# Optimization experiments

Measured on AMD Instinct MI355X. Metric: run time of the kernel, lower is better.

The kernel has to match this reference:

```python
import jax, jax.numpy as jnp
import numpy as np

B, L, D = 128, 512, 768   # batch, bert tokens, bert hidden
J = 32                    # clause boundaries -> S = J + 1 segments
S = J + 1
DM, DF = 200, 200         # transformer d_model / ffn dim
EPS = 1e-5


def _ln(x, g, b):
    m = x.mean(-1, keepdims=True)
    v = ((x - m) ** 2).mean(-1, keepdims=True)
    return (x - m) / jnp.sqrt(v + EPS) * g + b


def setup_inputs() -> dict:
    key = jax.random.key(0)
    ks = jax.random.split(key, 12)
    sc = 0.02
    hidden_state = jax.random.normal(ks[0], (B, L, D), jnp.float32)
    # strictly increasing, positive clause boundaries < L (non-empty segments)
    seg = L // S  # stride ~= 15 tokens per clause
    jitter = jax.random.randint(ks[1], (B, J), 0, seg).astype(jnp.int32)
    clause_idx = jnp.arange(1, J + 1, dtype=jnp.int32)[None, :] * seg + jitter
    p = lambda k, shp: sc * jax.random.normal(k, shp, jnp.float32)
    z = lambda n: jnp.zeros((n,), jnp.float32)
    return {
        'hidden_state': hidden_state,
        'clause_idx': clause_idx,
        'fc5_w': p(ks[2], (1, D)), 'fc5_b': z(1),
        'fc1_w': p(ks[3], (DM, D)), 'fc1_b': z(DM),
        'attn_in_w': p(ks[4], (3 * DM, DM)), 'attn_in_b': z(3 * DM),
        'attn_out_w': p(ks[5], (DM, DM)), 'attn_out_b': z(DM),
        'ln1_g': jnp.ones((DM,), jnp.float32), 'ln1_b': z(DM),
        'lin1_w': p(ks[6], (DF, DM)), 'lin1_b': z(DF),
        'lin2_w': p(ks[7], (DM, DF)), 'lin2_b': z(DM),
        'ln2_g': jnp.ones((DM,), jnp.float32), 'ln2_b': z(DM),
        'fc_w': p(ks[8], (2, 2 * DM)), 'fc_b': z(2),
    }


def reference(hidden_state, clause_idx, fc5_w, fc5_b, fc1_w, fc1_b,
              attn_in_w, attn_in_b, attn_out_w, attn_out_b,
              ln1_g, ln1_b, lin1_w, lin1_b, lin2_w, lin2_b,
              ln2_g, ln2_b, fc_w, fc_b):
    # ---- ragged per-segment attention pooling (batched_index_select) ----
    t = jnp.arange(L)
    # segment id of each token: number of boundaries <= t  -> [B, L] in [0, S)
    seg_id = jnp.sum(t[None, None, :] >= clause_idx[:, :, None], axis=1)
    scores = jnp.einsum('bld,d->bl', hidden_state, fc5_w[0]) + fc5_b[0]  # fc5
    mask = seg_id[:, None, :] == jnp.arange(S)[None, :, None]            # [B,S,L]
    logits = jnp.where(mask, scores[:, None, :], -jnp.inf)
    w = jax.nn.softmax(logits, axis=-1)        # per-segment softmax over tokens
    pooled = jnp.einsum('bsl,bld->bsd', w, hidden_state)                 # [B,S,D]

    # ---- fc1 + TransformerEncoderLayer (post-norm, 1 head, relu, no dropout)
    x = pooled @ fc1_w.T + fc1_b                                         # [B,S,DM]
    qkv = x @ attn_in_w.T + attn_in_b
    q, k, v = jnp.split(qkv, 3, axis=-1)
    a = jax.nn.softmax(jnp.einsum('bqd,bkd->bqk', q, k) * (1.0 / np.sqrt(DM).item()), axis=-1)
    att = jnp.einsum('bqk,bkd->bqd', a, v) @ attn_out_w.T + attn_out_b
    x = _ln(x + att, ln1_g, ln1_b)
    ff = jax.nn.relu(x @ lin1_w.T + lin1_b) @ lin2_w.T + lin2_b
    x = _ln(x + ff, ln2_g, ln2_b)

    # ---- cat(first-token broadcast, rest) then classifier fc ----
    h = jnp.concatenate([jnp.broadcast_to(x[:, :1, :], (B, S - 1, DM)), x[:, 1:, :]], axis=-1)
    return h @ fc_w.T + fc_b                                             # [B, S-1, 2]
```

## Files before the change

kernel.cpp:

```cpp
#include <hip/hip_runtime.h>

#define NB 128
#define LL 512
#define DD 768
#define JJ 32
#define SS 33
#define DM 200

typedef __attribute__((ext_vector_type(8))) short bf8_t;
typedef __attribute__((ext_vector_type(4))) float f4_t;

#define SB_XF   0
#define SB_QB   61440
#define SB_KB   82944
#define SB_VT   104448
#define SB_AB   131072
#define SB_Y2   235520
#define SB_BLK  275456

static __device__ __forceinline__ unsigned short f2bf(float f) {
  unsigned u = __float_as_uint(f);
  return (unsigned short)((u + 0x7FFFu + ((u >> 16) & 1u)) >> 16);
}

template<int KS>
static __device__ __forceinline__ f4_t mfma_tile(
    const unsigned short* pa, const unsigned short* pw)
{
  f4_t acc = {0.f, 0.f, 0.f, 0.f};
  bf8_t a = *(const bf8_t*)pa;
  bf8_t w = *(const bf8_t*)pw;
#pragma unroll
  for (int s = 1; s < KS; ++s) {
    bf8_t a2 = *(const bf8_t*)(pa + 32 * s);
    bf8_t w2 = *(const bf8_t*)(pw + 32 * s);
    acc = __builtin_amdgcn_mfma_f32_16x16x32_bf16(a, w, acc, 0, 0, 0);
    a = a2; w = w2;
  }
  acc = __builtin_amdgcn_mfma_f32_16x16x32_bf16(a, w, acc, 0, 0, 0);
  return acc;
}

template<int KS, int LDA>
static __device__ __forceinline__ f4_t mfma_tile_lds(
    const unsigned short* pa, const unsigned short* pw)
{
  f4_t acc = {0.f, 0.f, 0.f, 0.f};
#pragma unroll
  for (int s = 0; s < KS; ++s) {
    bf8_t a = *(const bf8_t*)(pa + 32 * s);
    bf8_t w = *(const bf8_t*)(pw + 32 * s);
    acc = __builtin_amdgcn_mfma_f32_16x16x32_bf16(a, w, acc, 0, 0, 0);
  }
  return acc;
}

__global__ __launch_bounds__(512) void pc_kernel(
    const float* __restrict__ hidden, const int* __restrict__ clause,
    const float* __restrict__ fc5w, unsigned short* __restrict__ pooled_bf,
    const float* __restrict__ fc1_w, const float* __restrict__ ain_w,
    const float* __restrict__ aout_w, const float* __restrict__ lin1_w,
    const float* __restrict__ lin2_w,
    unsigned short* __restrict__ fc1_wb, unsigned short* __restrict__ ain_wb,
    unsigned short* __restrict__ aout_wb, unsigned short* __restrict__ lin1_wb,
    unsigned short* __restrict__ lin2_wb, char* __restrict__ scratch)
{
  const int tid = threadIdx.x;
  if (blockIdx.x >= NB * SS) {
    int t = (blockIdx.x - NB * SS) * 512 + tid;
    if (t < 208 * 768) {
      int n = t / 768, k = t - n * 768;
      fc1_wb[t] = f2bf((n < 200) ? fc1_w[n * 768 + k] : 0.f);
      return;
    }
    t -= 208 * 768;
    if (t < 608 * 224) {
      int n = t / 224, k = t - n * 224;
      ain_wb[t] = f2bf((n < 600 && k < 200) ? ain_w[n * 200 + k] : 0.f);
      return;
    }
    t -= 608 * 224;
    if (t < 208 * 224) {
      int n = t / 224, k = t - n * 224;
      aout_wb[t] = f2bf((n < 200 && k < 200) ? aout_w[n * 200 + k] : 0.f);
      return;
    }
    t -= 208 * 224;
    if (t < 208 * 224) {
      int n = t / 224, k = t - n * 224;
      lin1_wb[t] = f2bf((n < 200 && k < 200) ? lin1_w[n * 200 + k] : 0.f);
      return;
    }
    t -= 208 * 224;
    if (t < 208 * 224) {
      int n = t / 224, k = t - n * 224;
      lin2_wb[t] = f2bf((n < 200 && k < 200) ? lin2_w[n * 200 + k] : 0.f);
      return;
    }
    t -= 208 * 224;
    if (t < NB * 1408) {
      int b = t / 1408, r = t - b * 1408;
      char* sb = scratch + (size_t)b * SB_BLK;
      const uint4 z = make_uint4(0, 0, 0, 0);
      if (r < 576) {
        int bi = r / 192, rr = r - bi * 192;
        int row = rr >> 2, c = rr & 3;
        int off = (bi == 0) ? SB_QB : (bi == 1 ? SB_KB : SB_AB);
        *(uint4*)((unsigned short*)(sb + off) + row * 224 + 192 + c * 8) = z;
      } else {
        int rr = r - 576;
        int row = rr >> 2, c = rr & 3;
        *(uint4*)((unsigned short*)(sb + SB_VT) + row * 64 + 32 + c * 8) = z;
      }
    }
    return;
  }

  int blk = blockIdx.x;
  int b = blk / SS;
  int s = blk - b * SS;
  int t0 = (s == 0) ? 0 : clause[b * JJ + s - 1];
  int t1 = (s == JJ) ? LL : clause[b * JJ + s];
  int nt = t1 - t0;
  if (nt > 64) nt = 64;
  if (nt < 1) nt = 1;

  __shared__ float wsm[64];
  int wave = tid >> 6, lane = tid & 63;

  const float4* w4 = (const float4*)fc5w;
  for (int t = t0 + wave; t < t0 + nt; t += 8) {
    const float4* hp = (const float4*)(hidden + ((long long)b * LL + t) * DD);
    float acc = 0.f;
#pragma unroll
    for (int i = 0; i < 3; ++i) {
      float4 h = hp[lane + 64 * i];
      float4 w = w4[lane + 64 * i];
      acc += h.x * w.x + h.y * w.y + h.z * w.z + h.w * w.w;
    }
#pragma unroll
    for (int off = 32; off; off >>= 1) acc += __shfl_xor(acc, off);
    if (lane == 0) wsm[t - t0] = acc;
  }
  __syncthreads();

  if (wave == 0) {
    float v = (lane < nt) ? wsm[lane] : -__builtin_inff();
    float mx = v;
#pragma unroll
    for (int off = 32; off; off >>= 1) mx = fmaxf(mx, __shfl_xor(mx, off));
    float e = (lane < nt) ? __expf(v - mx) : 0.f;
    float sm = e;
#pragma unroll
    for (int off = 32; off; off >>= 1) sm += __shfl_xor(sm, off);
    if (lane < nt) wsm[lane] = e / sm;
  }
  __syncthreads();

  if (tid < 384) {
    const float2* base = (const float2*)(hidden + ((long long)b * LL + t0) * DD);
    float2 acc = make_float2(0.f, 0.f);
#pragma unroll 4
    for (int t = 0; t < nt; ++t) {
      float w = wsm[t];
      float2 h = base[t * 384 + tid];
      acc.x = fmaf(w, h.x, acc.x);
      acc.y = fmaf(w, h.y, acc.y);
    }
    ushort2 o;
    o.x = f2bf(acc.x); o.y = f2bf(acc.y);
    *(ushort2*)(pooled_bf + (long long)blk * DD + tid * 2) = o;
  }
}

__global__ __launch_bounds__(256) void k_fc1qkv(
    const unsigned short* __restrict__ pooled,
    const unsigned short* __restrict__ fc1_wb, const float* __restrict__ fc1_b,
    const unsigned short* __restrict__ ain_wb, const float* __restrict__ ain_b,
    char* __restrict__ scratch)
{
  const int b = blockIdx.x / 3, mt = blockIdx.x % 3, m0 = mt * 16;
  const int tid = threadIdx.x, wv = tid >> 6, lane = tid & 63;
  const int col = lane & 15, quad = lane >> 4, koff = quad * 8;

  char* sb = scratch + (size_t)b * SB_BLK;
  float* x_f32 = (float*)(sb + SB_XF);
  unsigned short* q_bf  = (unsigned short*)(sb + SB_QB);
  unsigned short* k_bf  = (unsigned short*)(sb + SB_KB);
  unsigned short* vt_bf = (unsigned short*)(sb + SB_VT);

  __shared__ __align__(16) unsigned short xb[16][232];
  for (int u = tid; u < 16 * 16; u += 256) {
    int row = u >> 4, c = u & 15;
    ((unsigned*)&xb[row][200])[c] = 0u;
  }

  const unsigned short* Ab = pooled + (size_t)b * SS * DD;
  for (int t = wv; t < 13; t += 4) {
    int n0 = t * 16;
    f4_t acc = mfma_tile<24>(Ab + (size_t)(m0 + col) * DD + koff,
                             fc1_wb + (size_t)(n0 + col) * DD + koff);
    int gn = n0 + col;
    if (gn < DM) {
      float bv = fc1_b[gn];
#pragma unroll
      for (int r = 0; r < 4; ++r) {
        int row = quad * 4 + r;
        float v = acc[r] + bv;
        x_f32[(m0 + row) * 208 + gn] = v;
        xb[row][gn] = f2bf(v);
      }
    }
  }
  __syncthreads();

  for (int t = wv; t < 38; t += 4) {
    int n0 = t * 16;
    f4_t acc = mfma_tile_lds<7, 232>(&xb[0][0] + col * 232 + koff,
                                     ain_wb + (size_t)(n0 + col) * 224 + koff);
    int gn = n0 + col;
    if (gn < 600) {
      float bv = ain_b[gn];
#pragma unroll
      for (int r = 0; r < 4; ++r) {
        int gm = m0 + quad * 4 + r;
        unsigned short bfv = f2bf(acc[r] + bv);
        if (gn < 200)      q_bf[gm * 224 + gn] = bfv;
        else if (gn < 400) k_bf[gm * 224 + (gn - 200)] = bfv;
        else if (gm < SS)  vt_bf[(gn - 400) * 64 + gm] = bfv;
      }
    }
  }
}

__global__ __launch_bounds__(512) void k_attn(char* __restrict__ scratch)
{
  const int b = blockIdx.x, tid = threadIdx.x;
  const int wv = tid >> 6, lane = tid & 63;
  const int col = lane & 15, quad = lane >> 4, koff = quad * 8;

  char* sb = scratch + (size_t)b * SB_BLK;
  const unsigned short* q_bf  = (const unsigned short*)(sb + SB_QB);
  const unsigned short* k_bf  = (const unsigned short*)(sb + SB_KB);
  const unsigned short* vt_bf = (const unsigned short*)(sb + SB_VT);
  unsigned short* att_bf = (unsigned short*)(sb + SB_AB);

  __shared__ __align__(16) char smem[16896];
  float*          sc = (float*)smem;
  unsigned short* Pb = (unsigned short*)(smem + 9984);

  for (int t = wv; t < 9; t += 8) {
    int mt = t / 3, nt = t - mt * 3;
    int m0 = mt * 16, n0 = nt * 16;
    f4_t acc = mfma_tile<7>(q_bf + (m0 + col) * 224 + koff,
                            k_bf + (n0 + col) * 224 + koff);
    int gn = n0 + col;
#pragma unroll
    for (int r = 0; r < 4; ++r)
      sc[(m0 + quad * 4 + r) * 52 + gn] = acc[r] * 0.07071067811865475f;
  }
  __syncthreads();

  if (tid < SS) {
    float mx = -1e30f;
    for (int j = 0; j < SS; ++j) mx = fmaxf(mx, sc[tid * 52 + j]);
    float sm = 0.f;
    for (int j = 0; j < SS; ++j) { float e = __expf(sc[tid * 52 + j] - mx); sc[tid * 52 + j] = e; sm += e; }
    float inv = 1.f / sm;
    for (int j = 0; j < SS; ++j) sc[tid * 52 + j] *= inv;
  }
  __syncthreads();
  for (int u = tid; u < 48 * 64; u += 512) {
    int m = u >> 6, k = u & 63;
    Pb[m * 72 + k] = (m < SS && k < SS) ? f2bf(sc[m * 52 + k]) : (unsigned short)0;
  }
  __syncthreads();

  for (int t = wv; t < 3 * 13; t += 8) {
    int mt = t / 13, nt = t - mt * 13;
    int m0 = mt * 16, n0 = nt * 16;
    f4_t acc = mfma_tile_lds<2, 72>(Pb + (m0 + col) * 72 + koff,
                                    vt_bf + (n0 + col) * 64 + koff);
    int gn = n0 + col;
    if (gn < DM) {
#pragma unroll
      for (int r = 0; r < 4; ++r)
        att_bf[(m0 + quad * 4 + r) * 224 + gn] = f2bf(acc[r]);
    }
  }
}

__global__ __launch_bounds__(256) void k_post(
    const unsigned short* __restrict__ aout_wb, const float* __restrict__ aout_b,
    const float* __restrict__ ln1_g, const float* __restrict__ ln1_b,
    const unsigned short* __restrict__ lin1_wb, const float* __restrict__ lin1_b,
    const unsigned short* __restrict__ lin2_wb, const float* __restrict__ lin2_b,
    const float* __restrict__ ln2_g, const float* __restrict__ ln2_b,
    char* __restrict__ scratch)
{
  const int b = blockIdx.x / 3, mt = blockIdx.x % 3, m0 = mt * 16;
  const int tid = threadIdx.x, wv = tid >> 6, lane = tid & 63;
  const int col = lane & 15, quad = lane >> 4, koff = quad * 8;

  char* sb = scratch + (size_t)b * SB_BLK;
  const unsigned short* att_bf = (const unsigned short*)(sb + SB_AB);
  const float* x_f32 = (const float*)(sb + SB_XF);
  float* y2g = (float*)(sb + SB_Y2);

  __shared__ float tc[16][211];
  __shared__ __align__(16) unsigned short yb[16][232];
  __shared__ __align__(16) unsigned short fb[16][232];
  for (int u = tid; u < 16 * 16; u += 256) {
    int row = u >> 4, c = u & 15;
    ((unsigned*)&yb[row][200])[c] = 0u;
    ((unsigned*)&fb[row][200])[c] = 0u;
  }

  for (int t = wv; t < 13; t += 4) {
    int n0 = t * 16;
    f4_t acc = mfma_tile<7>(att_bf + (m0 + col) * 224 + koff,
                            aout_wb + (size_t)(n0 + col) * 224 + koff);
    int gn = n0 + col;
    float bv = (gn < DM) ? aout_b[gn] : 0.f;
#pragma unroll
    for (int r = 0; r < 4; ++r) {
      int row = quad * 4 + r;
      float v = acc[r] + bv;
      if (gn < DM) v += x_f32[(m0 + row) * 208 + gn];
      tc[row][gn] = v;
    }
  }
  __syncthreads();

  for (int r = wv; r < 16; r += 4) {
    float* p = &tc[r][0];
    float vals[4]; float s = 0.f;
#pragma unroll
    for (int i = 0; i < 4; ++i) { int k = lane + 64 * i; vals[i] = (k < DM) ? p[k] : 0.f; s += vals[i]; }
#pragma unroll
    for (int off = 32; off; off >>= 1) s += __shfl_xor(s, off);
    float mean = s * (1.f / DM);
    float vs = 0.f;
#pragma unroll
    for (int i = 0; i < 4; ++i) { int k = lane + 64 * i; if (k < DM) { float d = vals[i] - mean; vs += d * d; } }
#pragma unroll
    for (int off = 32; off; off >>= 1) vs += __shfl_xor(vs, off);
    float rstd = rsqrtf(vs * (1.f / DM) + 1e-5f);
#pragma unroll
    for (int i = 0; i < 4; ++i) {
      int k = lane + 64 * i;
      if (k < DM) {
        float o = (vals[i] - mean) * rstd * ln1_g[k] + ln1_b[k];
        p[k] = o;
        yb[r][k] = f2bf(o);
      }
    }
  }
  __syncthreads();

  for (int t = wv; t < 13; t += 4) {
    int n0 = t * 16;
    f4_t acc = mfma_tile_lds<7, 232>(&yb[0][0] + col * 232 + koff,
                                     lin1_wb + (size_t)(n0 + col) * 224 + koff);
    int gn = n0 + col;
    if (gn < DM) {
      float bv = lin1_b[gn];
#pragma unroll
      for (int r = 0; r < 4; ++r)
        fb[quad * 4 + r][gn] = f2bf(fmaxf(acc[r] + bv, 0.f));
    }
  }
  __syncthreads();

  for (int t = wv; t < 13; t += 4) {
    int n0 = t * 16;
    f4_t acc = mfma_tile_lds<7, 232>(&fb[0][0] + col * 232 + koff,
                                     lin2_wb + (size_t)(n0 + col) * 224 + koff);
    int gn = n0 + col;
    if (gn < DM) {
      float bv = lin2_b[gn];
#pragma unroll
      for (int r = 0; r < 4; ++r) {
        int row = quad * 4 + r;
        tc[row][gn] = acc[r] + bv + tc[row][gn];
      }
    }
  }
  __syncthreads();

  for (int r = wv; r < 16; r += 4) {
    float* p = &tc[r][0];
    float vals[4]; float s = 0.f;
#pragma unroll
    for (int i = 0; i < 4; ++i) { int k = lane + 64 * i; vals[i] = (k < DM) ? p[k] : 0.f; s += vals[i]; }
#pragma unroll
    for (int off = 32; off; off >>= 1) s += __shfl_xor(s, off);
    float mean = s * (1.f / DM);
    float vs = 0.f;
#pragma unroll
    for (int i = 0; i < 4; ++i) { int k = lane + 64 * i; if (k < DM) { float d = vals[i] - mean; vs += d * d; } }
#pragma unroll
    for (int off = 32; off; off >>= 1) vs += __shfl_xor(vs, off);
    float rstd = rsqrtf(vs * (1.f / DM) + 1e-5f);
    int grow = m0 + r;
#pragma unroll
    for (int i = 0; i < 4; ++i) {
      int k = lane + 64 * i;
      if (k < DM) y2g[grow * 208 + k] = (vals[i] - mean) * rstd * ln2_g[k] + ln2_b[k];
    }
  }
}

__global__ __launch_bounds__(256) void k_cls(
    const char* __restrict__ scratch, const float* __restrict__ fcw,
    const float* __restrict__ fcb, float* __restrict__ out)
{
  int gw = blockIdx.x * 4 + (threadIdx.x >> 6);
  int lane = threadIdx.x & 63;
  int b = gw >> 5, j = gw & 31;
  const float* y2 = (const float*)(scratch + (size_t)b * SB_BLK + SB_Y2);
  const float* r0 = y2;
  const float* rj = y2 + (1 + j) * 208;
  float a0 = 0.f, a1 = 0.f;
  for (int k = lane; k < DM; k += 64) {
    float u = r0[k], w = rj[k];
    a0 += u * fcw[k]       + w * fcw[200 + k];
    a1 += u * fcw[400 + k] + w * fcw[600 + k];
  }
#pragma unroll
  for (int off = 32; off; off >>= 1) {
    a0 += __shfl_xor(a0, off);
    a1 += __shfl_xor(a1, off);
  }
  if (lane == 0) {
    out[gw * 2 + 0] = a0 + fcb[0];
    out[gw * 2 + 1] = a1 + fcb[1];
  }
}

extern "C" void kernel_launch(void* const* d_in, const int* in_sizes, int n_in,
                              void* d_out, int out_size, void* d_ws, size_t ws_size,
                              hipStream_t stream)
{
  (void)in_sizes; (void)n_in; (void)out_size; (void)ws_size;
  const float* hidden = (const float*)d_in[0];
  const int*   clause = (const int*)d_in[1];
  const float* fc5_w  = (const float*)d_in[2];
  const float* fc1_w  = (const float*)d_in[4];
  const float* fc1_b  = (const float*)d_in[5];
  const float* ain_w  = (const float*)d_in[6];
  const float* ain_b  = (const float*)d_in[7];
  const float* aout_w = (const float*)d_in[8];
  const float* aout_b = (const float*)d_in[9];
  const float* ln1_g  = (const float*)d_in[10];
  const float* ln1_b  = (const float*)d_in[11];
  const float* lin1_w = (const float*)d_in[12];
  const float* lin1_b = (const float*)d_in[13];
  const float* lin2_w = (const float*)d_in[14];
  const float* lin2_b = (const float*)d_in[15];
  const float* ln2_g  = (const float*)d_in[16];
  const float* ln2_b  = (const float*)d_in[17];
  const float* fc_w   = (const float*)d_in[18];
  const float* fc_b   = (const float*)d_in[19];
  float* out = (float*)d_out;

  char* w8 = (char*)d_ws;
  unsigned short* pooled_bf = (unsigned short*)(w8 + 0);
  char* scratch = w8 + 6520832;
  size_t wbase = 6520832 + (size_t)NB * SB_BLK;
  unsigned short* fc1_wb  = (unsigned short*)(w8 + wbase);
  unsigned short* ain_wb  = (unsigned short*)(w8 + wbase + 319488);
  unsigned short* aout_wb = (unsigned short*)(w8 + wbase + 591872);
  unsigned short* lin1_wb = (unsigned short*)(w8 + wbase + 685056);
  unsigned short* lin2_wb = (unsigned short*)(w8 + wbase + 778240);

  pc_kernel<<<dim3(NB * SS + 1203), 512, 0, stream>>>(
      hidden, clause, fc5_w, pooled_bf,
      fc1_w, ain_w, aout_w, lin1_w, lin2_w,
      fc1_wb, ain_wb, aout_wb, lin1_wb, lin2_wb, scratch);
  k_fc1qkv<<<dim3(NB * 3), 256, 0, stream>>>(pooled_bf, fc1_wb, fc1_b,
      ain_wb, ain_b, scratch);
  k_attn<<<dim3(NB), 512, 0, stream>>>(scratch);
  k_post<<<dim3(NB * 3), 256, 0, stream>>>(aout_wb, aout_b, ln1_g, ln1_b,
      lin1_wb, lin1_b, lin2_wb, lin2_b, ln2_g, ln2_b, scratch);
  k_cls<<<dim3(1024), 256, 0, stream>>>(scratch, fc_w, fc_b, out);
}
```

Baseline: 397.0 us.

## Fuse attention into post-attention kernel and widen blocks to 512 threads

Removes the separate attention kernel. Each post-attention block now computes its 16-row slice of scores, does a wave-level softmax with shuffles, and multiplies by V directly in LDS. This drops one launch and the global round trip of the attention output buffer, and its zero-padding in the prep kernel. The fc1/qkv and post kernels also move from 256 to 512 threads so more waves share the MFMA tiles, at the cost of some idle waves in loops with 13 or fewer tiles.

```diff
diff --git a/kernel.cpp b/kernel.cpp
--- a/kernel.cpp
+++ b/kernel.cpp
@@ -14,7 +14,6 @@
 #define SB_QB   61440
 #define SB_KB   82944
 #define SB_VT   104448
-#define SB_AB   131072
 #define SB_Y2   235520
 #define SB_BLK  275456
 
@@ -41,7 +40,7 @@
   return acc;
 }
 
-template<int KS, int LDA>
+template<int KS>
 static __device__ __forceinline__ f4_t mfma_tile_lds(
     const unsigned short* pa, const unsigned short* pw)
 {
@@ -98,17 +97,17 @@
       return;
     }
     t -= 208 * 224;
-    if (t < NB * 1408) {
-      int b = t / 1408, r = t - b * 1408;
+    if (t < NB * 1344) {
+      int b = t / 1344, r = t - b * 1344;
       char* sb = scratch + (size_t)b * SB_BLK;
       const uint4 z = make_uint4(0, 0, 0, 0);
-      if (r < 576) {
+      if (r < 384) {
         int bi = r / 192, rr = r - bi * 192;
         int row = rr >> 2, c = rr & 3;
-        int off = (bi == 0) ? SB_QB : (bi == 1 ? SB_KB : SB_AB);
+        int off = (bi == 0) ? SB_QB : SB_KB;
         *(uint4*)((unsigned short*)(sb + off) + row * 224 + 192 + c * 8) = z;
       } else {
-        int rr = r - 576;
+        int rr = r - 384;
         int row = rr >> 2, c = rr & 3;
         *(uint4*)((unsigned short*)(sb + SB_VT) + row * 64 + 32 + c * 8) = z;
       }
@@ -173,7 +172,7 @@
   }
 }
 
-__global__ __launch_bounds__(256) void k_fc1qkv(
+__global__ __launch_bounds__(512) void k_fc1qkv(
     const unsigned short* __restrict__ pooled,
     const unsigned short* __restrict__ fc1_wb, const float* __restrict__ fc1_b,
     const unsigned short* __restrict__ ain_wb, const float* __restrict__ ain_b,
@@ -190,13 +189,13 @@
   unsigned short* vt_bf = (unsigned short*)(sb + SB_VT);
 
   __shared__ __align__(16) unsigned short xb[16][232];
-  for (int u = tid; u < 16 * 16; u += 256) {
+  for (int u = tid; u < 16 * 16; u += 512) {
     int row = u >> 4, c = u & 15;
     ((unsigned*)&xb[row][200])[c] = 0u;
   }
 
   const unsigned short* Ab = pooled + (size_t)b * SS * DD;
-  for (int t = wv; t < 13; t += 4) {
+  for (int t = wv; t < 13; t += 8) {
     int n0 = t * 16;
     f4_t acc = mfma_tile<24>(Ab + (size_t)(m0 + col) * DD + koff,
                              fc1_wb + (size_t)(n0 + col) * DD + koff);
@@ -214,10 +213,10 @@
   }
   __syncthreads();
 
-  for (int t = wv; t < 38; t += 4) {
-    int n0 = t * 16;
-    f4_t acc = mfma_tile_lds<7, 232>(&xb[0][0] + col * 232 + koff,
-                                     ain_wb + (size_t)(n0 + col) * 224 + koff);
+  for (int t = wv; t < 38; t += 8) {
+    int n0 = t * 16;
+    f4_t acc = mfma_tile_lds<7>(&xb[0][0] + col * 232 + koff,
+                                ain_wb + (size_t)(n0 + col) * 224 + koff);
     int gn = n0 + col;
     if (gn < 600) {
       float bv = ain_b[gn];
@@ -233,64 +232,7 @@
   }
 }
 
-__global__ __launch_bounds__(512) void k_attn(char* __restrict__ scratch)
-{
-  const int b = blockIdx.x, tid = threadIdx.x;
-  const int wv = tid >> 6, lane = tid & 63;
-  const int col = lane & 15, quad = lane >> 4, koff = quad * 8;
-
-  char* sb = scratch + (size_t)b * SB_BLK;
-  const unsigned short* q_bf  = (const unsigned short*)(sb + SB_QB);
-  const unsigned short* k_bf  = (const unsigned short*)(sb + SB_KB);
-  const unsigned short* vt_bf = (const unsigned short*)(sb + SB_VT);
-  unsigned short* att_bf = (unsigned short*)(sb + SB_AB);
-
-  __shared__ __align__(16) char smem[16896];
-  float*          sc = (float*)smem;
-  unsigned short* Pb = (unsigned short*)(smem + 9984);
-
-  for (int t = wv; t < 9; t += 8) {
-    int mt = t / 3, nt = t - mt * 3;
-    int m0 = mt * 16, n0 = nt * 16;
-    f4_t acc = mfma_tile<7>(q_bf + (m0 + col) * 224 + koff,
-                            k_bf + (n0 + col) * 224 + koff);
-    int gn = n0 + col;
-#pragma unroll
-    for (int r = 0; r < 4; ++r)
-      sc[(m0 + quad * 4 + r) * 52 + gn] = acc[r] * 0.07071067811865475f;
-  }
-  __syncthreads();
-
-  if (tid < SS) {
-    float mx = -1e30f;
-    for (int j = 0; j < SS; ++j) mx = fmaxf(mx, sc[tid * 52 + j]);
-    float sm = 0.f;
-    for (int j = 0; j < SS; ++j) { float e = __expf(sc[tid * 52 + j] - mx); sc[tid * 52 + j] = e; sm += e; }
-    float inv = 1.f / sm;
-    for (int j = 0; j < SS; ++j) sc[tid * 52 + j] *= inv;
-  }
-  __syncthreads();
-  for (int u = tid; u < 48 * 64; u += 512) {
-    int m = u >> 6, k = u & 63;
-    Pb[m * 72 + k] = (m < SS && k < SS) ? f2bf(sc[m * 52 + k]) : (unsigned short)0;
-  }
-  __syncthreads();
-
-  for (int t = wv; t < 3 * 13; t += 8) {
-    int mt = t / 13, nt = t - mt * 13;
-    int m0 = mt * 16, n0 = nt * 16;
-    f4_t acc = mfma_tile_lds<2, 72>(Pb + (m0 + col) * 72 + koff,
-                                    vt_bf + (n0 + col) * 64 + koff);
-    int gn = n0 + col;
-    if (gn < DM) {
-#pragma unroll
-      for (int r = 0; r < 4; ++r)
-        att_bf[(m0 + quad * 4 + r) * 224 + gn] = f2bf(acc[r]);
-    }
-  }
-}
-
-__global__ __launch_bounds__(256) void k_post(
+__global__ __launch_bounds__(512) void k_postattn(
     const unsigned short* __restrict__ aout_wb, const float* __restrict__ aout_b,
     const float* __restrict__ ln1_g, const float* __restrict__ ln1_b,
     const unsigned short* __restrict__ lin1_wb, const float* __restrict__ lin1_b,
@@ -303,23 +245,64 @@
   const int col = lane & 15, quad = lane >> 4, koff = quad * 8;
 
   char* sb = scratch + (size_t)b * SB_BLK;
-  const unsigned short* att_bf = (const unsigned short*)(sb + SB_AB);
+  const unsigned short* q_bf  = (const unsigned short*)(sb + SB_QB);
+  const unsigned short* k_bf  = (const unsigned short*)(sb + SB_KB);
+  const unsigned short* vt_bf = (const unsigned short*)(sb + SB_VT);
   const float* x_f32 = (const float*)(sb + SB_XF);
   float* y2g = (float*)(sb + SB_Y2);
 
   __shared__ float tc[16][211];
+  __shared__ __align__(16) unsigned short Pb[16][72];
   __shared__ __align__(16) unsigned short yb[16][232];
   __shared__ __align__(16) unsigned short fb[16][232];
-  for (int u = tid; u < 16 * 16; u += 256) {
+  for (int u = tid; u < 16 * 16; u += 512) {
     int row = u >> 4, c = u & 15;
     ((unsigned*)&yb[row][200])[c] = 0u;
     ((unsigned*)&fb[row][200])[c] = 0u;
   }
 
-  for (int t = wv; t < 13; t += 4) {
-    int n0 = t * 16;
-    f4_t acc = mfma_tile<7>(att_bf + (m0 + col) * 224 + koff,
-                            aout_wb + (size_t)(n0 + col) * 224 + koff);
+  for (int t = wv; t < 3; t += 8) {
+    int n0 = t * 16;
+    f4_t acc = mfma_tile<7>(q_bf + (m0 + col) * 224 + koff,
+                            k_bf + (n0 + col) * 224 + koff);
+    int gn = n0 + col;
+#pragma unroll
+    for (int r = 0; r < 4; ++r)
+      tc[quad * 4 + r][gn] = acc[r] * 0.07071067811865475f;
+  }
+  __syncthreads();
+
+  for (int r = wv; r < 16; r += 8) {
+    bool live = (m0 + r) < SS;
+    float v = (lane < SS && live) ? tc[r][lane] : -__builtin_inff();
+    float mx = v;
+#pragma unroll
+    for (int off = 32; off; off >>= 1) mx = fmaxf(mx, __shfl_xor(mx, off));
+    float e = (lane < SS && live) ? __expf(v - mx) : 0.f;
+    float sm = e;
+#pragma unroll
+    for (int off = 32; off; off >>= 1) sm += __shfl_xor(sm, off);
+    Pb[r][lane] = (lane < SS && live) ? f2bf(e / sm) : (unsigned short)0;
+  }
+  __syncthreads();
+
+  for (int t = wv; t < 13; t += 8) {
+    int n0 = t * 16;
+    f4_t acc = mfma_tile_lds<2>(&Pb[0][0] + col * 72 + koff,
+                                vt_bf + (n0 + col) * 64 + koff);
+    int gn = n0 + col;
+    if (gn < DM) {
+#pragma unroll
+      for (int r = 0; r < 4; ++r)
+        fb[quad * 4 + r][gn] = f2bf(acc[r]);
+    }
+  }
+  __syncthreads();
+
+  for (int t = wv; t < 13; t += 8) {
+    int n0 = t * 16;
+    f4_t acc = mfma_tile_lds<7>(&fb[0][0] + col * 232 + koff,
+                                aout_wb + (size_t)(n0 + col) * 224 + koff);
     int gn = n0 + col;
     float bv = (gn < DM) ? aout_b[gn] : 0.f;
 #pragma unroll
@@ -332,7 +315,7 @@
   }
   __syncthreads();
 
-  for (int r = wv; r < 16; r += 4) {
+  for (int r = wv; r < 16; r += 8) {
     float* p = &tc[r][0];
     float vals[4]; float s = 0.f;
 #pragma unroll
@@ -358,10 +341,10 @@
   }
   __syncthreads();
 
-  for (int t = wv; t < 13; t += 4) {
-    int n0 = t * 16;
-    f4_t acc = mfma_tile_lds<7, 232>(&yb[0][0] + col * 232 + koff,
-                                     lin1_wb + (size_t)(n0 + col) * 224 + koff);
+  for (int t = wv; t < 13; t += 8) {
+    int n0 = t * 16;
+    f4_t acc = mfma_tile_lds<7>(&yb[0][0] + col * 232 + koff,
+                                lin1_wb + (size_t)(n0 + col) * 224 + koff);
     int gn = n0 + col;
     if (gn < DM) {
       float bv = lin1_b[gn];
@@ -372,10 +355,10 @@
   }
   __syncthreads();
 
-  for (int t = wv; t < 13; t += 4) {
-    int n0 = t * 16;
-    f4_t acc = mfma_tile_lds<7, 232>(&fb[0][0] + col * 232 + koff,
-                                     lin2_wb + (size_t)(n0 + col) * 224 + koff);
+  for (int t = wv; t < 13; t += 8) {
+    int n0 = t * 16;
+    f4_t acc = mfma_tile_lds<7>(&fb[0][0] + col * 232 + koff,
+                                lin2_wb + (size_t)(n0 + col) * 224 + koff);
     int gn = n0 + col;
     if (gn < DM) {
       float bv = lin2_b[gn];
@@ -388,7 +371,7 @@
   }
   __syncthreads();
 
-  for (int r = wv; r < 16; r += 4) {
+  for (int r = wv; r < 16; r += 8) {
     float* p = &tc[r][0];
     float vals[4]; float s = 0.f;
 #pragma unroll
@@ -474,14 +457,13 @@
   unsigned short* lin1_wb = (unsigned short*)(w8 + wbase + 685056);
   unsigned short* lin2_wb = (unsigned short*)(w8 + wbase + 778240);
 
-  pc_kernel<<<dim3(NB * SS + 1203), 512, 0, stream>>>(
+  pc_kernel<<<dim3(NB * SS + 1187), 512, 0, stream>>>(
       hidden, clause, fc5_w, pooled_bf,
       fc1_w, ain_w, aout_w, lin1_w, lin2_w,
       fc1_wb, ain_wb, aout_wb, lin1_wb, lin2_wb, scratch);
-  k_fc1qkv<<<dim3(NB * 3), 256, 0, stream>>>(pooled_bf, fc1_wb, fc1_b,
+  k_fc1qkv<<<dim3(NB * 3), 512, 0, stream>>>(pooled_bf, fc1_wb, fc1_b,
       ain_wb, ain_b, scratch);
-  k_attn<<<dim3(NB), 512, 0, stream>>>(scratch);
-  k_post<<<dim3(NB * 3), 256, 0, stream>>>(aout_wb, aout_b, ln1_g, ln1_b,
+  k_postattn<<<dim3(NB * 3), 512, 0, stream>>>(aout_wb, aout_b, ln1_g, ln1_b,
       lin1_wb, lin1_b, lin2_wb, lin2_b, ln2_g, ln2_b, scratch);
   k_cls<<<dim3(1024), 256, 0, stream>>>(scratch, fc_w, fc_b, out);
 }
```

Result: faster. 382.1 us (-3.8%).
